# Performance work log

Measured on AMD Instinct MI355X. Metric: run time of the kernel, lower is better.

## Reference

```python
import jax, jax.numpy as jnp
import numpy as np

N_HEAD = 16


def setup_inputs() -> dict:
    key = jax.random.key(0)
    ks = jax.random.split(key, 6)
    B, S, D = 2, 2048, 1024
    w = 0.02
    return {
        "x": jax.random.normal(ks[0], (B, S, D), dtype=jnp.float32),
        "attention_mask": jnp.ones((B, S), dtype=jnp.int32),
        "Wq": jax.random.normal(ks[1], (D, D), dtype=jnp.float32) * w,
        "bq": jnp.zeros((D,), dtype=jnp.float32),
        "Wk": jax.random.normal(ks[2], (D, D), dtype=jnp.float32) * w,
        "bk": jnp.zeros((D,), dtype=jnp.float32),
        "Wv": jax.random.normal(ks[3], (D, D), dtype=jnp.float32) * w,
        "bv": jnp.zeros((D,), dtype=jnp.float32),
        "Wp": jax.random.normal(ks[4], (D, D), dtype=jnp.float32) * w,
        "bp": jnp.zeros((D,), dtype=jnp.float32),
    }


def reference(x, attention_mask, Wq, bq, Wk, bk, Wv, bv, Wp, bp):
    # x: (B,S,D); PyTorch Linear: y = x @ W.T + b
    B, S, D = x.shape
    H = N_HEAD
    HD = D // H
    scale = 1.0 / jnp.sqrt(jnp.asarray(HD, dtype=x.dtype))

    def heads(W, b):
        return (x @ W.T + b).reshape(B, S, H, HD).transpose(0, 2, 1, 3)  # (B,H,S,HD)

    q = heads(Wq, bq)
    k = heads(Wk, bk)
    v = heads(Wv, bv)

    logits = jnp.einsum("bhsd,bhtd->bhst", q, k) * scale  # (B,H,S,S)

    causal = jnp.tril(jnp.ones((S, S), dtype=bool))  # (S,S)
    am = attention_mask.astype(bool)
    mask = causal[None, None, :, :] & (am[:, None, :, None] & am[:, None, None, :])

    float_min = jnp.finfo(x.dtype).min
    logits = jnp.where(mask, logits, float_min)
    w = jax.nn.softmax(logits, axis=-1)  # dropout is identity in eval / p=0

    attn = jnp.einsum("bhst,bhtd->bhsd", w, v)  # (B,H,S,HD)
    attn = attn.transpose(0, 2, 1, 3).reshape(B, S, D)
    return attn @ Wp.T + bp
```

## Files before the change

### kernel.cpp

```cpp
#include <hip/hip_runtime.h>


#define BB 2
#define SS 2048
#define DD 1024
#define HH 16
#define HDD 64
#define NEG_BIG (-1.0e30f)
#define QSCL 0.18033688011112042f

typedef __attribute__((ext_vector_type(8))) short short8;
typedef __attribute__((ext_vector_type(4))) float floatx4;
typedef unsigned int u32;
#define AS_GLOBAL __attribute__((address_space(1)))
#define AS_LDS    __attribute__((address_space(3)))

__device__ __forceinline__ ushort f2bf(float f) {
    unsigned u = __float_as_uint(f);
    u += 0x7fffu + ((u >> 16) & 1u);
    return (ushort)(u >> 16);
}
__device__ __forceinline__ unsigned pk2(float a, float b) {
    return ((unsigned)f2bf(b) << 16) | (unsigned)f2bf(a);
}
__device__ __forceinline__ unsigned cvtpk(float a, float b) {
    unsigned r;
    asm("v_cvt_pk_bf16_f32 %0, %1, %2" : "=v"(r) : "v"(a), "v"(b));
    return r;
}
__device__ __forceinline__ void unpack8(const uint4 u, float* d) {
    d[0] = __uint_as_float(u.x << 16);
    d[1] = __uint_as_float(u.x & 0xffff0000u);
    d[2] = __uint_as_float(u.y << 16);
    d[3] = __uint_as_float(u.y & 0xffff0000u);
    d[4] = __uint_as_float(u.z << 16);
    d[5] = __uint_as_float(u.z & 0xffff0000u);
    d[6] = __uint_as_float(u.w << 16);
    d[7] = __uint_as_float(u.w & 0xffff0000u);
}
__device__ __forceinline__ void dma16(void* lds, const void* g) {
    __builtin_amdgcn_global_load_lds((const AS_GLOBAL u32*)g, (AS_LDS u32*)lds,
                                     16, 0, 0);
}

__global__ __launch_bounds__(256) void cvt_all(
    const float* __restrict__ x, const float* __restrict__ wq,
    const float* __restrict__ wk, const float* __restrict__ wv,
    ushort* __restrict__ dst)
{
    const size_t flat = ((size_t)blockIdx.x * 256 + threadIdx.x) * 8;
    const float* s;
    size_t off;
    float scl = 1.0f;
    if (flat < (size_t)4194304)      { s = x;  off = flat; }
    else if (flat < (size_t)5242880) { s = wq; off = flat - 4194304; scl = QSCL; }
    else if (flat < (size_t)6291456) { s = wk; off = flat - 5242880; }
    else                             { s = wv; off = flat - 6291456; }
    const float4 a = ((const float4*)(s + off))[0];
    const float4 b = ((const float4*)(s + off))[1];
    uint4 u;
    u.x = pk2(a.x * scl, a.y * scl); u.y = pk2(a.z * scl, a.w * scl);
    u.z = pk2(b.x * scl, b.y * scl); u.w = pk2(b.z * scl, b.w * scl);
    *(uint4*)(dst + flat) = u;
}

template <int MODE, typename TW, typename TO>
__global__ __launch_bounds__(256) void gemm_mfma(
    const ushort* __restrict__ A,
    const TW* __restrict__ W0, const TW* __restrict__ W1,
    const float* __restrict__ B0, const float* __restrict__ B1,
    TO* __restrict__ O0, TO* __restrict__ O1)
{
    __shared__ ushort As[128 * 32];
    __shared__ ushort Bs[128 * 32];
    __shared__ float bias_s[128];

    const TW* W = W0;
    const float* bias = B0;
    TO* out = O0;
    if (MODE == 1 && blockIdx.z == 1) { W = W1; bias = B1; out = O1; }

    const int tid = threadIdx.x;
    const int bm = blockIdx.x * 128, bn = blockIdx.y * 128;
    const int wave = tid >> 6, lane = tid & 63, quad = lane >> 4, lm = lane & 15;
    const int wm = wave >> 1, wn = wave & 1;
    const int r0 = tid >> 2, c0 = (tid & 3) * 8;

    if (tid < 128) {
        float bb = bias[bn + tid];
        if (MODE == 1 && blockIdx.z == 0) bb *= QSCL;
        bias_s[tid] = bb;
    }

    const floatx4 zz = {0.f, 0.f, 0.f, 0.f};
    floatx4 acc[4][4];
#pragma unroll
    for (int i = 0; i < 4; ++i)
#pragma unroll
        for (int j = 0; j < 4; ++j) acc[i][j] = zz;

    for (int k0 = 0; k0 < DD; k0 += 32) {
        __syncthreads();
        dma16(&As[r0 * 32 + c0], A + (size_t)(bm + r0) * DD + k0 + c0);
        dma16(&As[(64 + r0) * 32 + c0], A + (size_t)(bm + 64 + r0) * DD + k0 + c0);
        if constexpr (sizeof(TW) == 2) {
            dma16(&Bs[r0 * 32 + c0],
                  (const ushort*)W + (size_t)(bn + r0) * DD + k0 + c0);
            dma16(&Bs[(64 + r0) * 32 + c0],
                  (const ushort*)W + (size_t)(bn + 64 + r0) * DD + k0 + c0);
        } else {
#pragma unroll
            for (int hh = 0; hh < 2; ++hh) {
                const float* wr = (const float*)W
                    + (size_t)(bn + hh * 64 + r0) * DD + k0 + c0;
                const float4 a = ((const float4*)wr)[0];
                const float4 b = ((const float4*)wr)[1];
                uint4 u;
                u.x = pk2(a.x, a.y); u.y = pk2(a.z, a.w);
                u.z = pk2(b.x, b.y); u.w = pk2(b.z, b.w);
                *(uint4*)&Bs[(hh * 64 + r0) * 32 + c0] = u;
            }
        }
        __syncthreads();

        short8 af[4], bf[4];
#pragma unroll
        for (int i = 0; i < 4; ++i)
            af[i] = *(const short8*)&As[(wm * 64 + i * 16 + lm) * 32 + quad * 8];
#pragma unroll
        for (int j = 0; j < 4; ++j)
            bf[j] = *(const short8*)&Bs[(wn * 64 + j * 16 + lm) * 32 + quad * 8];
#pragma unroll
        for (int i = 0; i < 4; ++i)
#pragma unroll
            for (int j = 0; j < 4; ++j) {
                if (MODE == 2)
                    acc[i][j] = __builtin_amdgcn_mfma_f32_16x16x32_bf16(
                        af[i], bf[j], acc[i][j], 0, 0, 0);
                else
                    acc[i][j] = __builtin_amdgcn_mfma_f32_16x16x32_bf16(
                        bf[j], af[i], acc[i][j], 0, 0, 0);
            }
    }

#pragma unroll
    for (int i = 0; i < 4; ++i) {
#pragma unroll
        for (int j = 0; j < 4; ++j) {
            if (MODE == 2) {
                const int n = bn + wn * 64 + j * 16 + lm;
                const int m0 = bm + wm * 64 + i * 16 + quad * 4;
                const int b = m0 >> 11, s0 = m0 & 2047;
                const float bb = bias_s[n - bn];
                ushort4 v;
                v.x = f2bf(acc[i][j][0] + bb);
                v.y = f2bf(acc[i][j][1] + bb);
                v.z = f2bf(acc[i][j][2] + bb);
                v.w = f2bf(acc[i][j][3] + bb);
                *(ushort4*)((ushort*)out + ((size_t)(b * DD + n)) * SS + s0) = v;
            } else {
                const int nl = wn * 64 + j * 16 + quad * 4;
                const int n = bn + nl;
                const int m = bm + wm * 64 + i * 16 + lm;
                if (MODE == 1) {
                    const int b = m >> 11, s = m & 2047, h = n >> 6, hd = n & 63;
                    ushort4 v;
                    v.x = f2bf(acc[i][j][0] + bias_s[nl + 0]);
                    v.y = f2bf(acc[i][j][1] + bias_s[nl + 1]);
                    v.z = f2bf(acc[i][j][2] + bias_s[nl + 2]);
                    v.w = f2bf(acc[i][j][3] + bias_s[nl + 3]);
                    *(ushort4*)((ushort*)out
                        + (((size_t)(b * HH + h) * SS) + s) * HDD + hd) = v;
                } else {
                    float4 v;
                    v.x = acc[i][j][0] + bias_s[nl + 0];
                    v.y = acc[i][j][1] + bias_s[nl + 1];
                    v.z = acc[i][j][2] + bias_s[nl + 2];
                    v.w = acc[i][j][3] + bias_s[nl + 3];
                    *(float4*)((float*)out + (size_t)m * DD + n) = v;
                }
            }
        }
    }
}

__global__ __launch_bounds__(256) void attn_mfma(
    const ushort* __restrict__ Q, const ushort* __restrict__ K,
    const ushort* __restrict__ Vt, const int* __restrict__ am,
    ushort* __restrict__ Opart, float* __restrict__ lbuf)
{
    __shared__ ushort Ks[64 * 72];
    __shared__ ushort Vts[64 * 72];
    __shared__ ushort Ps[4][32 * 72];
    __shared__ int amk_s[64];

    const int tid = threadIdx.x;
    const int wq = tid >> 6, lane = tid & 63, quad = lane >> 4, lm = lane & 15;
    const int bh = blockIdx.y, b = bh >> 4, h = bh & 15;
    const int qt = b ? (int)blockIdx.x : (int)(gridDim.x - 1 - blockIdx.x);
    const int split = blockIdx.z;
    const size_t base = (size_t)bh * SS * HDD;
    const size_t tbase = (size_t)bh * HDD * SS;
    const int* amrow = am + b * SS;
    const int q0 = qt * 128 + wq * 32;

    short8 qf[2][2];
#pragma unroll
    for (int sub = 0; sub < 2; ++sub) {
        const ushort* qp = Q + base + (size_t)(q0 + sub * 16 + lm) * HDD + quad * 8;
        qf[sub][0] = *(const short8*)qp;
        qf[sub][1] = *(const short8*)(qp + 32);
    }
    int amq[2];
#pragma unroll
    for (int sub = 0; sub < 2; ++sub) amq[sub] = amrow[q0 + sub * 16 + lm];
    const bool allq = __all(amq[0] != 0 && amq[1] != 0);

    const floatx4 zz = {0.f, 0.f, 0.f, 0.f};
    floatx4 o_acc[2][4];
#pragma unroll
    for (int sub = 0; sub < 2; ++sub)
#pragma unroll
        for (int n2 = 0; n2 < 4; ++n2) o_acc[sub][n2] = zz;
    float l_lane[2] = {0.f, 0.f};

    const int sr = tid >> 2, sc = (tid & 3) * 16;
    const int ktmax = 2 * qt + 1;

    uint4 kra, krb, vra, vrb;
    int amr = 1;
    {
        const ushort* kp = K + base + (size_t)(split * 64 + sr) * HDD + sc;
        kra = ((const uint4*)kp)[0]; krb = ((const uint4*)kp)[1];
        const ushort* vp = Vt + tbase + (size_t)sr * SS + split * 64 + sc;
        vra = ((const uint4*)vp)[0]; vrb = ((const uint4*)vp)[1];
        if (tid < 64) amr = amrow[split * 64 + tid];
    }
    *(uint4*)&Ks[sr * 72 + sc] = kra;
    *(uint4*)&Ks[sr * 72 + sc + 8] = krb;
    *(uint4*)&Vts[sr * 72 + sc] = vra;
    *(uint4*)&Vts[sr * 72 + sc + 8] = vrb;
    if (tid < 64) amk_s[tid] = amr;
    __syncthreads();

    for (int kt = split; kt <= ktmax; kt += 2) {
        const int nxt = kt + 2;
        const bool have_nxt = nxt <= ktmax;
        if (have_nxt) {
            const ushort* kp = K + base + (size_t)(nxt * 64 + sr) * HDD + sc;
            kra = ((const uint4*)kp)[0]; krb = ((const uint4*)kp)[1];
            const ushort* vp = Vt + tbase + (size_t)sr * SS + nxt * 64 + sc;
            vra = ((const uint4*)vp)[0]; vrb = ((const uint4*)vp)[1];
            if (tid < 64) amr = amrow[nxt * 64 + tid];
        }

        const bool allk = (__ballot(amk_s[lane] != 0) == ~0ull);
        const bool fast = allk & allq & ((kt * 64 + 63) <= q0);
        if (fast) {
#pragma unroll
            for (int nt = 0; nt < 4; ++nt) {
                const short8 kf0 = *(const short8*)&Ks[(nt * 16 + lm) * 72 + quad * 8];
                const short8 kf1 = *(const short8*)&Ks[(nt * 16 + lm) * 72 + 32 + quad * 8];
#pragma unroll
                for (int sub = 0; sub < 2; ++sub) {
                    floatx4 s = zz;
                    s = __builtin_amdgcn_mfma_f32_16x16x32_bf16(kf0, qf[sub][0], s, 0, 0, 0);
                    s = __builtin_amdgcn_mfma_f32_16x16x32_bf16(kf1, qf[sub][1], s, 0, 0, 0);
                    const float e0 = exp2f(fminf(s[0], 40.f));
                    const float e1 = exp2f(fminf(s[1], 40.f));
                    const float e2 = exp2f(fminf(s[2], 40.f));
                    const float e3 = exp2f(fminf(s[3], 40.f));
                    l_lane[sub] += (e0 + e1) + (e2 + e3);
                    uint2 pv;
                    pv.x = cvtpk(e0, e1); pv.y = cvtpk(e2, e3);
                    *(uint2*)&Ps[wq][(sub * 16 + lm) * 72 + nt * 16 + quad * 4] = pv;
                }
            }
        } else {
#pragma unroll
            for (int nt = 0; nt < 4; ++nt) {
                const short8 kf0 = *(const short8*)&Ks[(nt * 16 + lm) * 72 + quad * 8];
                const short8 kf1 = *(const short8*)&Ks[(nt * 16 + lm) * 72 + 32 + quad * 8];
                const int4 amk4 = *(const int4*)&amk_s[nt * 16 + quad * 4];
#pragma unroll
                for (int sub = 0; sub < 2; ++sub) {
                    floatx4 s = zz;
                    s = __builtin_amdgcn_mfma_f32_16x16x32_bf16(kf0, qf[sub][0], s, 0, 0, 0);
                    s = __builtin_amdgcn_mfma_f32_16x16x32_bf16(kf1, qf[sub][1], s, 0, 0, 0);
                    const int qg = q0 + sub * 16 + lm;
                    const int t0 = kt * 64 + nt * 16 + quad * 4;
                    const bool mq = amq[sub] != 0;
                    const bool ok0 = amk4.x && mq && (t0 + 0 <= qg);
                    const bool ok1 = amk4.y && mq && (t0 + 1 <= qg);
                    const bool ok2 = amk4.z && mq && (t0 + 2 <= qg);
                    const bool ok3 = amk4.w && mq && (t0 + 3 <= qg);
                    const float e0 = exp2f(fminf(ok0 ? s[0] : NEG_BIG, 40.f));
                    const float e1 = exp2f(fminf(ok1 ? s[1] : NEG_BIG, 40.f));
                    const float e2 = exp2f(fminf(ok2 ? s[2] : NEG_BIG, 40.f));
                    const float e3 = exp2f(fminf(ok3 ? s[3] : NEG_BIG, 40.f));
                    l_lane[sub] += (e0 + e1) + (e2 + e3);
                    uint2 pv;
                    pv.x = cvtpk(e0, e1); pv.y = cvtpk(e2, e3);
                    *(uint2*)&Ps[wq][(sub * 16 + lm) * 72 + nt * 16 + quad * 4] = pv;
                }
            }
        }

        short8 af[2][2];
#pragma unroll
        for (int sub = 0; sub < 2; ++sub) {
            af[sub][0] = *(const short8*)&Ps[wq][(sub * 16 + lm) * 72 + quad * 8];
            af[sub][1] = *(const short8*)&Ps[wq][(sub * 16 + lm) * 72 + 32 + quad * 8];
        }
#pragma unroll
        for (int n2 = 0; n2 < 4; ++n2) {
            const short8 vf0 = *(const short8*)&Vts[(n2 * 16 + lm) * 72 + quad * 8];
            const short8 vf1 = *(const short8*)&Vts[(n2 * 16 + lm) * 72 + 32 + quad * 8];
#pragma unroll
            for (int sub = 0; sub < 2; ++sub) {
                o_acc[sub][n2] = __builtin_amdgcn_mfma_f32_16x16x32_bf16(
                    vf0, af[sub][0], o_acc[sub][n2], 0, 0, 0);
                o_acc[sub][n2] = __builtin_amdgcn_mfma_f32_16x16x32_bf16(
                    vf1, af[sub][1], o_acc[sub][n2], 0, 0, 0);
            }
        }

        if (have_nxt) {
            __syncthreads();
            *(uint4*)&Ks[sr * 72 + sc] = kra;
            *(uint4*)&Ks[sr * 72 + sc + 8] = krb;
            *(uint4*)&Vts[sr * 72 + sc] = vra;
            *(uint4*)&Vts[sr * 72 + sc + 8] = vrb;
            if (tid < 64) amk_s[tid] = amr;
            __syncthreads();
        }
    }

#pragma unroll
    for (int sub = 0; sub < 2; ++sub) {
        float l = l_lane[sub];
        l += __shfl_xor(l, 16);
        l += __shfl_xor(l, 32);
        if (quad == 0)
            lbuf[(size_t)split * (BB * HH * SS) + (size_t)bh * SS + q0 + sub * 16 + lm] = l;
        const int srow = q0 + sub * 16 + lm;
#pragma unroll
        for (int n2 = 0; n2 < 4; ++n2) {
            uint2 v;
            v.x = cvtpk(o_acc[sub][n2][0], o_acc[sub][n2][1]);
            v.y = cvtpk(o_acc[sub][n2][2], o_acc[sub][n2][3]);
            *(uint2*)(Opart + (size_t)split * (BB * SS * DD)
                        + ((size_t)(b * SS + srow)) * DD + h * HDD + n2 * 16 + quad * 4) = v;
        }
    }
}

__global__ __launch_bounds__(256) void combine(
    const ushort* __restrict__ Opart, const float* __restrict__ lbuf,
    ushort* __restrict__ Aout)
{
    const size_t e = ((size_t)blockIdx.x * 256 + threadIdx.x) * 8;
    const int m = (int)(e >> 10);
    const int col = (int)(e & 1023);
    const int b = m >> 11, s = m & 2047, h = col >> 6;
    const float l = lbuf[(b * HH + h) * SS + s]
                  + lbuf[BB * HH * SS + (b * HH + h) * SS + s];
    const float inv = l > 0.f ? 1.f / l : 0.f;
    const uint4 u0 = *(const uint4*)(Opart + e);
    const uint4 u1 = *(const uint4*)(Opart + (size_t)BB * SS * DD + e);
    float f0[8], f1[8];
    unpack8(u0, f0);
    unpack8(u1, f1);
    uint4 o;
    o.x = pk2((f0[0] + f1[0]) * inv, (f0[1] + f1[1]) * inv);
    o.y = pk2((f0[2] + f1[2]) * inv, (f0[3] + f1[3]) * inv);
    o.z = pk2((f0[4] + f1[4]) * inv, (f0[5] + f1[5]) * inv);
    o.w = pk2((f0[6] + f1[6]) * inv, (f0[7] + f1[7]) * inv);
    *(uint4*)(Aout + e) = o;
}

extern "C" void kernel_launch(void* const* d_in, const int* in_sizes, int n_in,
                              void* d_out, int out_size, void* d_ws, size_t ws_size,
                              hipStream_t stream) {
    const float* x  = (const float*)d_in[0];
    const int*   am = (const int*)d_in[1];
    const float* Wq = (const float*)d_in[2];
    const float* bq = (const float*)d_in[3];
    const float* Wk = (const float*)d_in[4];
    const float* bk = (const float*)d_in[5];
    const float* Wv = (const float*)d_in[6];
    const float* bv = (const float*)d_in[7];
    const float* Wp = (const float*)d_in[8];
    const float* bp = (const float*)d_in[9];
    float* out = (float*)d_out;

    const size_t elems = (size_t)BB * HH * SS * HDD;
    ushort* q_ws = (ushort*)d_ws;
    ushort* k_ws = q_ws + elems;
    ushort* v_ws = k_ws + elems;
    float*  lbuf = (float*)(v_ws + elems);

    ushort* xb  = (ushort*)d_out;
    ushort* wqb = xb + 4194304;
    ushort* wkb = wqb + 1048576;
    ushort* wvb = wkb + 1048576;

    cvt_all<<<3584, 256, 0, stream>>>(x, Wq, Wk, Wv, xb);

    gemm_mfma<1, ushort, ushort><<<dim3(32, 8, 2), 256, 0, stream>>>(
        xb, wqb, wkb, bq, bk, q_ws, k_ws);
    gemm_mfma<2, ushort, ushort><<<dim3(32, 8, 1), 256, 0, stream>>>(
        xb, wvb, (const ushort*)nullptr, bv, (const float*)nullptr,
        v_ws, (ushort*)nullptr);

    attn_mfma<<<dim3(SS / 128, BB * HH, 2), 256, 0, stream>>>(
        q_ws, k_ws, v_ws, am, (ushort*)d_out, lbuf);

    combine<<<2048, 256, 0, stream>>>((const ushort*)d_out, lbuf, q_ws);

    gemm_mfma<0, float, float><<<dim3(32, 8, 1), 256, 0, stream>>>(
        q_ws, Wp, (const float*)nullptr, bp, (const float*)nullptr,
        out, (float*)nullptr);
}
```

Before: 236.9 us.

## Use single-wave attention blocks reading K/V directly from global memory

Restructures the attention kernel from 256-thread blocks that staged K and V tiles in LDS, with register prefetch and block barriers, into 64-thread single-wave blocks. Each wave loads K and V fragments straight from global memory and keeps only its private P tile in LDS. This removes the barriers and LDS staging and gives finer-grained work per block for causal load balance. In exchange, K/V reuse across the four waves of a block is lost, so global/L2 traffic rises, and the explicit prefetch overlap is gone.

```diff
diff --git a/kernel.cpp b/kernel.cpp
--- a/kernel.cpp
+++ b/kernel.cpp
@@ -184,25 +184,22 @@
     }
 }
 
-__global__ __launch_bounds__(256) void attn_mfma(
+__global__ __launch_bounds__(64, 5) void attn_mfma(
     const ushort* __restrict__ Q, const ushort* __restrict__ K,
     const ushort* __restrict__ Vt, const int* __restrict__ am,
     ushort* __restrict__ Opart, float* __restrict__ lbuf)
 {
-    __shared__ ushort Ks[64 * 72];
-    __shared__ ushort Vts[64 * 72];
-    __shared__ ushort Ps[4][32 * 72];
-    __shared__ int amk_s[64];
-
-    const int tid = threadIdx.x;
-    const int wq = tid >> 6, lane = tid & 63, quad = lane >> 4, lm = lane & 15;
+    __shared__ ushort Ps[32 * 72];
+
+    const int lane = threadIdx.x;
+    const int quad = lane >> 4, lm = lane & 15;
     const int bh = blockIdx.y, b = bh >> 4, h = bh & 15;
-    const int qt = b ? (int)blockIdx.x : (int)(gridDim.x - 1 - blockIdx.x);
+    const int c = (int)(gridDim.x - 1 - blockIdx.x);
     const int split = blockIdx.z;
     const size_t base = (size_t)bh * SS * HDD;
     const size_t tbase = (size_t)bh * HDD * SS;
     const int* amrow = am + b * SS;
-    const int q0 = qt * 128 + wq * 32;
+    const int q0 = c * 32;
 
     short8 qf[2][2];
 #pragma unroll
@@ -224,43 +221,20 @@
         for (int n2 = 0; n2 < 4; ++n2) o_acc[sub][n2] = zz;
     float l_lane[2] = {0.f, 0.f};
 
-    const int sr = tid >> 2, sc = (tid & 3) * 16;
-    const int ktmax = 2 * qt + 1;
-
-    uint4 kra, krb, vra, vrb;
-    int amr = 1;
-    {
-        const ushort* kp = K + base + (size_t)(split * 64 + sr) * HDD + sc;
-        kra = ((const uint4*)kp)[0]; krb = ((const uint4*)kp)[1];
-        const ushort* vp = Vt + tbase + (size_t)sr * SS + split * 64 + sc;
-        vra = ((const uint4*)vp)[0]; vrb = ((const uint4*)vp)[1];
-        if (tid < 64) amr = amrow[split * 64 + tid];
-    }
-    *(uint4*)&Ks[sr * 72 + sc] = kra;
-    *(uint4*)&Ks[sr * 72 + sc + 8] = krb;
-    *(uint4*)&Vts[sr * 72 + sc] = vra;
-    *(uint4*)&Vts[sr * 72 + sc + 8] = vrb;
-    if (tid < 64) amk_s[tid] = amr;
-    __syncthreads();
+    const int ktmax = (q0 + 31) >> 6;
 
     for (int kt = split; kt <= ktmax; kt += 2) {
-        const int nxt = kt + 2;
-        const bool have_nxt = nxt <= ktmax;
-        if (have_nxt) {
-            const ushort* kp = K + base + (size_t)(nxt * 64 + sr) * HDD + sc;
-            kra = ((const uint4*)kp)[0]; krb = ((const uint4*)kp)[1];
-            const ushort* vp = Vt + tbase + (size_t)sr * SS + nxt * 64 + sc;
-            vra = ((const uint4*)vp)[0]; vrb = ((const uint4*)vp)[1];
-            if (tid < 64) amr = amrow[nxt * 64 + tid];
-        }
-
-        const bool allk = (__ballot(amk_s[lane] != 0) == ~0ull);
+        const int amv = amrow[kt * 64 + lane];
+        const bool allk = (__ballot(amv != 0) == ~0ull);
         const bool fast = allk & allq & ((kt * 64 + 63) <= q0);
+
         if (fast) {
 #pragma unroll
             for (int nt = 0; nt < 4; ++nt) {
-                const short8 kf0 = *(const short8*)&Ks[(nt * 16 + lm) * 72 + quad * 8];
-                const short8 kf1 = *(const short8*)&Ks[(nt * 16 + lm) * 72 + 32 + quad * 8];
+                const ushort* kp =
+                    K + base + (size_t)(kt * 64 + nt * 16 + lm) * HDD + quad * 8;
+                const short8 kf0 = *(const short8*)kp;
+                const short8 kf1 = *(const short8*)(kp + 32);
 #pragma unroll
                 for (int sub = 0; sub < 2; ++sub) {
                     floatx4 s = zz;
@@ -273,15 +247,18 @@
                     l_lane[sub] += (e0 + e1) + (e2 + e3);
                     uint2 pv;
                     pv.x = cvtpk(e0, e1); pv.y = cvtpk(e2, e3);
-                    *(uint2*)&Ps[wq][(sub * 16 + lm) * 72 + nt * 16 + quad * 4] = pv;
+                    *(uint2*)&Ps[(sub * 16 + lm) * 72 + nt * 16 + quad * 4] = pv;
                 }
             }
         } else {
 #pragma unroll
             for (int nt = 0; nt < 4; ++nt) {
-                const short8 kf0 = *(const short8*)&Ks[(nt * 16 + lm) * 72 + quad * 8];
-                const short8 kf1 = *(const short8*)&Ks[(nt * 16 + lm) * 72 + 32 + quad * 8];
-                const int4 amk4 = *(const int4*)&amk_s[nt * 16 + quad * 4];
+                const ushort* kp =
+                    K + base + (size_t)(kt * 64 + nt * 16 + lm) * HDD + quad * 8;
+                const short8 kf0 = *(const short8*)kp;
+                const short8 kf1 = *(const short8*)(kp + 32);
+                const int4 amk4 =
+                    *(const int4*)(amrow + kt * 64 + nt * 16 + quad * 4);
 #pragma unroll
                 for (int sub = 0; sub < 2; ++sub) {
                     floatx4 s = zz;
@@ -301,7 +278,7 @@
                     l_lane[sub] += (e0 + e1) + (e2 + e3);
                     uint2 pv;
                     pv.x = cvtpk(e0, e1); pv.y = cvtpk(e2, e3);
-                    *(uint2*)&Ps[wq][(sub * 16 + lm) * 72 + nt * 16 + quad * 4] = pv;
+                    *(uint2*)&Ps[(sub * 16 + lm) * 72 + nt * 16 + quad * 4] = pv;
                 }
             }
         }
@@ -309,13 +286,15 @@
         short8 af[2][2];
 #pragma unroll
         for (int sub = 0; sub < 2; ++sub) {
-            af[sub][0] = *(const short8*)&Ps[wq][(sub * 16 + lm) * 72 + quad * 8];
-            af[sub][1] = *(const short8*)&Ps[wq][(sub * 16 + lm) * 72 + 32 + quad * 8];
+            af[sub][0] = *(const short8*)&Ps[(sub * 16 + lm) * 72 + quad * 8];
+            af[sub][1] = *(const short8*)&Ps[(sub * 16 + lm) * 72 + 32 + quad * 8];
         }
 #pragma unroll
         for (int n2 = 0; n2 < 4; ++n2) {
-            const short8 vf0 = *(const short8*)&Vts[(n2 * 16 + lm) * 72 + quad * 8];
-            const short8 vf1 = *(const short8*)&Vts[(n2 * 16 + lm) * 72 + 32 + quad * 8];
+            const ushort* vp =
+                Vt + tbase + (size_t)(n2 * 16 + lm) * SS + kt * 64 + quad * 8;
+            const short8 vf0 = *(const short8*)vp;
+            const short8 vf1 = *(const short8*)(vp + 32);
 #pragma unroll
             for (int sub = 0; sub < 2; ++sub) {
                 o_acc[sub][n2] = __builtin_amdgcn_mfma_f32_16x16x32_bf16(
@@ -323,16 +302,6 @@
                 o_acc[sub][n2] = __builtin_amdgcn_mfma_f32_16x16x32_bf16(
                     vf1, af[sub][1], o_acc[sub][n2], 0, 0, 0);
             }
-        }
-
-        if (have_nxt) {
-            __syncthreads();
-            *(uint4*)&Ks[sr * 72 + sc] = kra;
-            *(uint4*)&Ks[sr * 72 + sc + 8] = krb;
-            *(uint4*)&Vts[sr * 72 + sc] = vra;
-            *(uint4*)&Vts[sr * 72 + sc + 8] = vrb;
-            if (tid < 64) amk_s[tid] = amr;
-            __syncthreads();
         }
     }
 
@@ -413,7 +382,7 @@
         xb, wvb, (const ushort*)nullptr, bv, (const float*)nullptr,
         v_ws, (ushort*)nullptr);
 
-    attn_mfma<<<dim3(SS / 128, BB * HH, 2), 256, 0, stream>>>(
+    attn_mfma<<<dim3(64, BB * HH, 2), 64, 0, stream>>>(
         q_ws, k_ws, v_ws, am, (ushort*)d_out, lbuf);
 
     combine<<<2048, 256, 0, stream>>>((const ushort*)d_out, lbuf, q_ws);
```

Result: slower. 319.5 us (+34.9%).

## Register-prefetch GEMM tiles, fuse Q/K GEMMs, pre-convert Wp to bf16

Applied to the files above, without the earlier changes.

Replaces the direct global-to-LDS DMA GEMM with a register-staged version that loads the next K tile while MFMAs run on the current one. Q and K projections now share a single A tile per block, computing two weight products at once. Wp is converted to bf16 in the conversion kernel rather than inside the output GEMM. This trades extra registers and LDS (launch bounds set to two blocks per SM) and halves the block count of the Q/K GEMM, which reduces parallelism.

```diff
diff --git a/kernel.cpp b/kernel.cpp
--- a/kernel.cpp
+++ b/kernel.cpp
@@ -12,8 +12,6 @@
 typedef __attribute__((ext_vector_type(8))) short short8;
 typedef __attribute__((ext_vector_type(4))) float floatx4;
 typedef unsigned int u32;
-#define AS_GLOBAL __attribute__((address_space(1)))
-#define AS_LDS    __attribute__((address_space(3)))
 
 __device__ __forceinline__ ushort f2bf(float f) {
     unsigned u = __float_as_uint(f);
@@ -38,47 +36,41 @@
     d[6] = __uint_as_float(u.w << 16);
     d[7] = __uint_as_float(u.w & 0xffff0000u);
 }
-__device__ __forceinline__ void dma16(void* lds, const void* g) {
-    __builtin_amdgcn_global_load_lds((const AS_GLOBAL u32*)g, (AS_LDS u32*)lds,
-                                     16, 0, 0);
-}
 
 __global__ __launch_bounds__(256) void cvt_all(
     const float* __restrict__ x, const float* __restrict__ wq,
     const float* __restrict__ wk, const float* __restrict__ wv,
-    ushort* __restrict__ dst)
+    const float* __restrict__ wp,
+    ushort* __restrict__ dst, ushort* __restrict__ wp_dst)
 {
     const size_t flat = ((size_t)blockIdx.x * 256 + threadIdx.x) * 8;
     const float* s;
+    ushort* d = dst + flat;
     size_t off;
     float scl = 1.0f;
     if (flat < (size_t)4194304)      { s = x;  off = flat; }
     else if (flat < (size_t)5242880) { s = wq; off = flat - 4194304; scl = QSCL; }
     else if (flat < (size_t)6291456) { s = wk; off = flat - 5242880; }
-    else                             { s = wv; off = flat - 6291456; }
+    else if (flat < (size_t)7340032) { s = wv; off = flat - 6291456; }
+    else { s = wp; off = flat - 7340032; d = wp_dst + off; }
     const float4 a = ((const float4*)(s + off))[0];
     const float4 b = ((const float4*)(s + off))[1];
     uint4 u;
     u.x = pk2(a.x * scl, a.y * scl); u.y = pk2(a.z * scl, a.w * scl);
     u.z = pk2(b.x * scl, b.y * scl); u.w = pk2(b.z * scl, b.w * scl);
-    *(uint4*)(dst + flat) = u;
-}
-
-template <int MODE, typename TW, typename TO>
-__global__ __launch_bounds__(256) void gemm_mfma(
+    *(uint4*)d = u;
+}
+
+template <int NW, int MODE, typename TO>
+__global__ __launch_bounds__(256, 2) void gemm_pipe(
     const ushort* __restrict__ A,
-    const TW* __restrict__ W0, const TW* __restrict__ W1,
+    const ushort* __restrict__ W0, const ushort* __restrict__ W1,
     const float* __restrict__ B0, const float* __restrict__ B1,
     TO* __restrict__ O0, TO* __restrict__ O1)
 {
     __shared__ ushort As[128 * 32];
-    __shared__ ushort Bs[128 * 32];
-    __shared__ float bias_s[128];
-
-    const TW* W = W0;
-    const float* bias = B0;
-    TO* out = O0;
-    if (MODE == 1 && blockIdx.z == 1) { W = W1; bias = B1; out = O1; }
+    __shared__ ushort Bs[NW][128 * 32];
+    __shared__ float bias_s[NW][128];
 
     const int tid = threadIdx.x;
     const int bm = blockIdx.x * 128, bn = blockIdx.y * 128;
@@ -87,97 +79,130 @@
     const int r0 = tid >> 2, c0 = (tid & 3) * 8;
 
     if (tid < 128) {
-        float bb = bias[bn + tid];
-        if (MODE == 1 && blockIdx.z == 0) bb *= QSCL;
-        bias_s[tid] = bb;
+        float b0 = B0[bn + tid];
+        if (MODE == 1) b0 *= QSCL;
+        bias_s[0][tid] = b0;
+        if (NW == 2) bias_s[1][tid] = B1[bn + tid];
     }
 
     const floatx4 zz = {0.f, 0.f, 0.f, 0.f};
-    floatx4 acc[4][4];
-#pragma unroll
-    for (int i = 0; i < 4; ++i)
-#pragma unroll
-        for (int j = 0; j < 4; ++j) acc[i][j] = zz;
+    floatx4 acc[NW][4][4];
+#pragma unroll
+    for (int w = 0; w < NW; ++w)
+#pragma unroll
+        for (int i = 0; i < 4; ++i)
+#pragma unroll
+            for (int j = 0; j < 4; ++j) acc[w][i][j] = zz;
+
+    const ushort* ap = A + (size_t)(bm + r0) * DD + c0;
+    const ushort* w0p = W0 + (size_t)(bn + r0) * DD + c0;
+    const ushort* w1p = (NW == 2) ? (W1 + (size_t)(bn + r0) * DD + c0) : W0;
+
+    uint4 ar0, ar1, wr0a, wr0b, wr1a, wr1b;
+
+#define LOADT(K0)                                                          \
+    do {                                                                   \
+        ar0 = *(const uint4*)(ap + (K0));                                  \
+        ar1 = *(const uint4*)(ap + (size_t)64 * DD + (K0));                \
+        wr0a = *(const uint4*)(w0p + (K0));                                \
+        wr0b = *(const uint4*)(w0p + (size_t)64 * DD + (K0));              \
+        if (NW == 2) {                                                     \
+            wr1a = *(const uint4*)(w1p + (K0));                            \
+            wr1b = *(const uint4*)(w1p + (size_t)64 * DD + (K0));          \
+        }                                                                  \
+    } while (0)
+
+#define STORET()                                                           \
+    do {                                                                   \
+        *(uint4*)&As[r0 * 32 + c0] = ar0;                                  \
+        *(uint4*)&As[(64 + r0) * 32 + c0] = ar1;                           \
+        *(uint4*)&Bs[0][r0 * 32 + c0] = wr0a;                              \
+        *(uint4*)&Bs[0][(64 + r0) * 32 + c0] = wr0b;                       \
+        if (NW == 2) {                                                     \
+            *(uint4*)&Bs[1][r0 * 32 + c0] = wr1a;                          \
+            *(uint4*)&Bs[1][(64 + r0) * 32 + c0] = wr1b;                   \
+        }                                                                  \
+    } while (0)
+
+    LOADT(0);
+    STORET();
+    __syncthreads();
 
     for (int k0 = 0; k0 < DD; k0 += 32) {
-        __syncthreads();
-        dma16(&As[r0 * 32 + c0], A + (size_t)(bm + r0) * DD + k0 + c0);
-        dma16(&As[(64 + r0) * 32 + c0], A + (size_t)(bm + 64 + r0) * DD + k0 + c0);
-        if constexpr (sizeof(TW) == 2) {
-            dma16(&Bs[r0 * 32 + c0],
-                  (const ushort*)W + (size_t)(bn + r0) * DD + k0 + c0);
-            dma16(&Bs[(64 + r0) * 32 + c0],
-                  (const ushort*)W + (size_t)(bn + 64 + r0) * DD + k0 + c0);
-        } else {
-#pragma unroll
-            for (int hh = 0; hh < 2; ++hh) {
-                const float* wr = (const float*)W
-                    + (size_t)(bn + hh * 64 + r0) * DD + k0 + c0;
-                const float4 a = ((const float4*)wr)[0];
-                const float4 b = ((const float4*)wr)[1];
-                uint4 u;
-                u.x = pk2(a.x, a.y); u.y = pk2(a.z, a.w);
-                u.z = pk2(b.x, b.y); u.w = pk2(b.z, b.w);
-                *(uint4*)&Bs[(hh * 64 + r0) * 32 + c0] = u;
-            }
-        }
-        __syncthreads();
-
-        short8 af[4], bf[4];
+        const bool have_nxt = (k0 + 32) < DD;
+        if (have_nxt) LOADT(k0 + 32);
+
+        short8 af[4];
 #pragma unroll
         for (int i = 0; i < 4; ++i)
             af[i] = *(const short8*)&As[(wm * 64 + i * 16 + lm) * 32 + quad * 8];
 #pragma unroll
-        for (int j = 0; j < 4; ++j)
-            bf[j] = *(const short8*)&Bs[(wn * 64 + j * 16 + lm) * 32 + quad * 8];
-#pragma unroll
-        for (int i = 0; i < 4; ++i)
+        for (int w = 0; w < NW; ++w) {
+            short8 bf[4];
+#pragma unroll
+            for (int j = 0; j < 4; ++j)
+                bf[j] = *(const short8*)&Bs[w][(wn * 64 + j * 16 + lm) * 32 + quad * 8];
+#pragma unroll
+            for (int i = 0; i < 4; ++i)
+#pragma unroll
+                for (int j = 0; j < 4; ++j) {
+                    if (MODE == 2)
+                        acc[w][i][j] = __builtin_amdgcn_mfma_f32_16x16x32_bf16(
+                            af[i], bf[j], acc[w][i][j], 0, 0, 0);
+                    else
+                        acc[w][i][j] = __builtin_amdgcn_mfma_f32_16x16x32_bf16(
+                            bf[j], af[i], acc[w][i][j], 0, 0, 0);
+                }
+        }
+
+        if (have_nxt) {
+            __syncthreads();
+            STORET();
+            __syncthreads();
+        }
+    }
+#undef LOADT
+#undef STORET
+
+#pragma unroll
+    for (int w = 0; w < NW; ++w) {
+        TO* out = (w == 0) ? O0 : O1;
+#pragma unroll
+        for (int i = 0; i < 4; ++i) {
 #pragma unroll
             for (int j = 0; j < 4; ++j) {
-                if (MODE == 2)
-                    acc[i][j] = __builtin_amdgcn_mfma_f32_16x16x32_bf16(
-                        af[i], bf[j], acc[i][j], 0, 0, 0);
-                else
-                    acc[i][j] = __builtin_amdgcn_mfma_f32_16x16x32_bf16(
-                        bf[j], af[i], acc[i][j], 0, 0, 0);
-            }
-    }
-
-#pragma unroll
-    for (int i = 0; i < 4; ++i) {
-#pragma unroll
-        for (int j = 0; j < 4; ++j) {
-            if (MODE == 2) {
-                const int n = bn + wn * 64 + j * 16 + lm;
-                const int m0 = bm + wm * 64 + i * 16 + quad * 4;
-                const int b = m0 >> 11, s0 = m0 & 2047;
-                const float bb = bias_s[n - bn];
-                ushort4 v;
-                v.x = f2bf(acc[i][j][0] + bb);
-                v.y = f2bf(acc[i][j][1] + bb);
-                v.z = f2bf(acc[i][j][2] + bb);
-                v.w = f2bf(acc[i][j][3] + bb);
-                *(ushort4*)((ushort*)out + ((size_t)(b * DD + n)) * SS + s0) = v;
-            } else {
-                const int nl = wn * 64 + j * 16 + quad * 4;
-                const int n = bn + nl;
-                const int m = bm + wm * 64 + i * 16 + lm;
-                if (MODE == 1) {
-                    const int b = m >> 11, s = m & 2047, h = n >> 6, hd = n & 63;
+                if (MODE == 2) {
+                    const int n = bn + wn * 64 + j * 16 + lm;
+                    const int m0 = bm + wm * 64 + i * 16 + quad * 4;
+                    const int b = m0 >> 11, s0 = m0 & 2047;
+                    const float bb = bias_s[0][n - bn];
                     ushort4 v;
-                    v.x = f2bf(acc[i][j][0] + bias_s[nl + 0]);
-                    v.y = f2bf(acc[i][j][1] + bias_s[nl + 1]);
-                    v.z = f2bf(acc[i][j][2] + bias_s[nl + 2]);
-                    v.w = f2bf(acc[i][j][3] + bias_s[nl + 3]);
-                    *(ushort4*)((ushort*)out
-                        + (((size_t)(b * HH + h) * SS) + s) * HDD + hd) = v;
+                    v.x = f2bf(acc[w][i][j][0] + bb);
+                    v.y = f2bf(acc[w][i][j][1] + bb);
+                    v.z = f2bf(acc[w][i][j][2] + bb);
+                    v.w = f2bf(acc[w][i][j][3] + bb);
+                    *(ushort4*)((ushort*)out + ((size_t)(b * DD + n)) * SS + s0) = v;
                 } else {
-                    float4 v;
-                    v.x = acc[i][j][0] + bias_s[nl + 0];
-                    v.y = acc[i][j][1] + bias_s[nl + 1];
-                    v.z = acc[i][j][2] + bias_s[nl + 2];
-                    v.w = acc[i][j][3] + bias_s[nl + 3];
-                    *(float4*)((float*)out + (size_t)m * DD + n) = v;
+                    const int nl = wn * 64 + j * 16 + quad * 4;
+                    const int n = bn + nl;
+                    const int m = bm + wm * 64 + i * 16 + lm;
+                    if (MODE == 1) {
+                        const int b = m >> 11, s = m & 2047, h = n >> 6, hd = n & 63;
+                        ushort4 v;
+                        v.x = f2bf(acc[w][i][j][0] + bias_s[w][nl + 0]);
+                        v.y = f2bf(acc[w][i][j][1] + bias_s[w][nl + 1]);
+                        v.z = f2bf(acc[w][i][j][2] + bias_s[w][nl + 2]);
+                        v.w = f2bf(acc[w][i][j][3] + bias_s[w][nl + 3]);
+                        *(ushort4*)((ushort*)out
+                            + (((size_t)(b * HH + h) * SS) + s) * HDD + hd) = v;
+                    } else {
+                        float4 v;
+                        v.x = acc[w][i][j][0] + bias_s[0][nl + 0];
+                        v.y = acc[w][i][j][1] + bias_s[0][nl + 1];
+                        v.z = acc[w][i][j][2] + bias_s[0][nl + 2];
+                        v.w = acc[w][i][j][3] + bias_s[0][nl + 3];
+                        *(float4*)((float*)out + (size_t)m * DD + n) = v;
+                    }
                 }
             }
         }
@@ -399,17 +424,18 @@
     ushort* k_ws = q_ws + elems;
     ushort* v_ws = k_ws + elems;
     float*  lbuf = (float*)(v_ws + elems);
+    ushort* wpb  = (ushort*)(lbuf + 2 * BB * HH * SS);
 
     ushort* xb  = (ushort*)d_out;
     ushort* wqb = xb + 4194304;
     ushort* wkb = wqb + 1048576;
     ushort* wvb = wkb + 1048576;
 
-    cvt_all<<<3584, 256, 0, stream>>>(x, Wq, Wk, Wv, xb);
-
-    gemm_mfma<1, ushort, ushort><<<dim3(32, 8, 2), 256, 0, stream>>>(
+    cvt_all<<<4096, 256, 0, stream>>>(x, Wq, Wk, Wv, Wp, xb, wpb);
+
+    gemm_pipe<2, 1, ushort><<<dim3(32, 8), 256, 0, stream>>>(
         xb, wqb, wkb, bq, bk, q_ws, k_ws);
-    gemm_mfma<2, ushort, ushort><<<dim3(32, 8, 1), 256, 0, stream>>>(
+    gemm_pipe<1, 2, ushort><<<dim3(32, 8), 256, 0, stream>>>(
         xb, wvb, (const ushort*)nullptr, bv, (const float*)nullptr,
         v_ws, (ushort*)nullptr);
 
@@ -418,7 +444,7 @@
 
     combine<<<2048, 256, 0, stream>>>((const ushort*)d_out, lbuf, q_ws);
 
-    gemm_mfma<0, float, float><<<dim3(32, 8, 1), 256, 0, stream>>>(
-        q_ws, Wp, (const float*)nullptr, bp, (const float*)nullptr,
+    gemm_pipe<1, 0, float><<<dim3(32, 8), 256, 0, stream>>>(
+        q_ws, wpb, (const ushort*)nullptr, bp, (const float*)nullptr,
         out, (float*)nullptr);
 }
```

Measured after the change: 219.4 us. 7.4% less time.
